# Kernel optimization log

Hardware: AMD Instinct MI355X
Metric: run time of the kernel (lower is better)

The kernel has to match this reference:

```python
import jax, jax.numpy as jnp
import numpy as np

N_NODES = 100000
N_EDGES = 1600000


def setup_inputs() -> dict:
    key = jax.random.key(0)
    k1, k2, k3, k4 = jax.random.split(key, 4)
    x = jax.random.normal(k1, (N_NODES, 16), dtype=jnp.float32)
    edge_index = jax.random.randint(k2, (2, N_EDGES), 0, N_NODES, dtype=jnp.int32)
    # Glorot-ish init for the two GCN layers
    W1 = jax.random.normal(k3, (16, 32), dtype=jnp.float32) * (1.0 / np.sqrt(16))
    b1 = jnp.zeros((32,), dtype=jnp.float32)
    W2 = jax.random.normal(k4, (32, 2), dtype=jnp.float32) * (1.0 / np.sqrt(32))
    b2 = jnp.zeros((2,), dtype=jnp.float32)
    return {"x": x, "edge_index": edge_index, "W1": W1, "b1": b1, "W2": W2, "b2": b2}


def _gcn_conv(x, W, b, src, dst, norm, n_nodes):
    # PyG GCNConv: h = X @ W; aggregate norm * h[src] at dst; add bias.
    h = x @ W                                   # [N, out]
    msg = h[src] * norm[:, None]                # [E+N, out] gather + scale
    out = jax.ops.segment_sum(msg, dst, num_segments=n_nodes)
    return out + b


def reference(x, edge_index, W1, b1, W2, b2):
    n = x.shape[0]
    self_loops = jnp.arange(n, dtype=edge_index.dtype)
    src = jnp.concatenate([edge_index[0], self_loops])  # [E+N]
    dst = jnp.concatenate([edge_index[1], self_loops])
    # Symmetric GCN normalization: deg computed on graph with self-loops
    deg = jax.ops.segment_sum(jnp.ones_like(dst, dtype=x.dtype), dst, num_segments=n)
    dis = jnp.where(deg > 0, jax.lax.rsqrt(deg), 0.0)   # deg^{-1/2}
    norm = dis[src] * dis[dst]                          # [E+N]

    h = jax.nn.relu(_gcn_conv(x, W1, b1, src, dst, norm, n))
    out = _gcn_conv(h, W2, b2, src, dst, norm, n)
    return out
```

## Files before the change

### kernel.cpp

```cpp
#include <hip/hip_runtime.h>
#include <hip/hip_fp16.h>

static constexpr int N  = 100000;
static constexpr int E  = 1600000;
static constexpr int B  = 256;
static constexpr int BG = 512;

static constexpr int BC     = 1024;
static constexpr int NBLKC  = 256;
static constexpr int CHUNKC = E / NBLKC;
static constexpr int PERC   = (CHUNKC + BC - 1) / BC;
static constexpr int NBUCK  = (N + 127) / 128;
static constexpr int SLAB   = 3072;
static constexpr int GCS    = 16;


__global__ __launch_bounds__(BC) void kC_scatter(
        const int* __restrict__ src, const int* __restrict__ dst,
        int* __restrict__ gcur, int* __restrict__ gslab) {
    __shared__ int lhist[NBUCK];
    __shared__ int lbase[NBUCK];
    __shared__ int gb[NBUCK];
    __shared__ int wsum[16];
    __shared__ int stage[CHUNKC];

    int t = threadIdx.x, blk = blockIdx.x;
    for (int i = t; i < NBUCK; i += BC) lhist[i] = 0;
    __syncthreads();

    int eb = blk * CHUNKC;
    int ds[PERC], ss[PERC];
#pragma unroll
    for (int k = 0; k < PERC; ++k) {
        int idx = k * BC + t;
        if (idx < CHUNKC) {
            ds[k] = dst[eb + idx];
            ss[k] = src[eb + idx];
            atomicAdd(&lhist[ds[k] >> 7], 1);
        }
    }
    __syncthreads();

    int lane = t & 63, wv = t >> 6;
    int val = (t < NBUCK) ? lhist[t] : 0;
    int inc = val;
#pragma unroll
    for (int off = 1; off < 64; off <<= 1) {
        int u = __shfl_up(inc, off, 64);
        if (lane >= off) inc += u;
    }
    if (lane == 63) wsum[wv] = inc;
    __syncthreads();
    if (wv == 0) {
        int wval = (lane < 16) ? wsum[lane] : 0;
        int winc = wval;
#pragma unroll
        for (int off = 1; off < 16; off <<= 1) {
            int u = __shfl_up(winc, off, 64);
            if (lane >= off) winc += u;
        }
        if (lane < 16) wsum[lane] = winc - wval;
    }
    __syncthreads();
    if (t < NBUCK) lbase[t] = wsum[wv] + inc - val;
    __syncthreads();

    if (t < NBUCK) {
        int h = lhist[t];
        if (h > 0) gb[t] = t * SLAB + atomicAdd(&gcur[t * GCS], h);
        lhist[t] = 0;
    }
    __syncthreads();

#pragma unroll
    for (int k = 0; k < PERC; ++k) {
        int idx = k * BC + t;
        if (idx < CHUNKC) {
            int d = ds[k], b = d >> 7;
            int r = atomicAdd(&lhist[b], 1);
            stage[lbase[b] + r] = ss[k] | ((d & 127) << 17);
        }
    }
    __syncthreads();

    if (t < NBUCK) {
        int len = lhist[t];
        if (len > 0) {
            int s0 = lbase[t];
            int g  = gb[t];
            int cap = (t + 1) * SLAB - g;
            if (cap < 0) cap = 0;
            if (len > cap) len = cap;
            for (int i = 0; i < len; ++i) gslab[g + i] = stage[s0 + i];
        }
    }
}


__global__ void kD1_deg(const int* __restrict__ gcur, const int* __restrict__ gslab,
                        int* __restrict__ rofs, const float4* __restrict__ x4,
                        __half* __restrict__ xpre) {
    __shared__ int c[128];
    __shared__ int wq[2];
    int t = threadIdx.x, b = blockIdx.x;
    if (t < 128) c[t] = 0;
    __syncthreads();

    int ne = min(gcur[b * GCS], SLAB);
    int base = b * SLAB;
    int ne4 = ne & ~3;
    for (int k = 4 * t; k < ne4; k += 4 * B) {
        int4 p4 = *(const int4*)(gslab + base + k);
        atomicAdd(&c[p4.x >> 17], 1);
        atomicAdd(&c[p4.y >> 17], 1);
        atomicAdd(&c[p4.z >> 17], 1);
        atomicAdd(&c[p4.w >> 17], 1);
    }
    if (t < ne - ne4) atomicAdd(&c[gslab[base + ne4 + t] >> 17], 1);
    __syncthreads();

    int lane = t & 63, wv = t >> 6;
    int val = (t < 128) ? c[t] : 0;
    int inc = val;
#pragma unroll
    for (int off = 1; off < 64; off <<= 1) {
        int u = __shfl_up(inc, off, 64);
        if (lane >= off) inc += u;
    }
    if (t == 63) wq[0] = inc;
    __syncthreads();
    if (t < 128) rofs[b * 129 + t] = base + inc - val + ((wv == 1) ? wq[0] : 0);
    if (t == 128) rofs[b * 129 + 128] = base + ne;

    int n = b * 128 + (t >> 1), h = t & 1;
    if (n < N) {
        float d = rsqrtf((float)(c[t >> 1] + 1));
        float4 u0 = x4[(size_t)n * 4 + h * 2];
        float4 u1 = x4[(size_t)n * 4 + h * 2 + 1];
        ushort4 p0, p1;
        p0.x = __half_as_ushort(__float2half(u0.x * d));
        p0.y = __half_as_ushort(__float2half(u0.y * d));
        p0.z = __half_as_ushort(__float2half(u0.z * d));
        p0.w = __half_as_ushort(__float2half(u0.w * d));
        p1.x = __half_as_ushort(__float2half(u1.x * d));
        p1.y = __half_as_ushort(__float2half(u1.y * d));
        p1.z = __half_as_ushort(__float2half(u1.z * d));
        p1.w = __half_as_ushort(__float2half(u1.w * d));
        *(ushort4*)(xpre + (size_t)n * 16 + h * 8)     = p0;
        *(ushort4*)(xpre + (size_t)n * 16 + h * 8 + 4) = p1;
    }
}


__global__ __launch_bounds__(BG) void kD2_agg(
        const __half* __restrict__ xpre, int* __restrict__ gslab,
        const int* __restrict__ rofs, const float* __restrict__ W1,
        const float* __restrict__ b1, const float* __restrict__ W2,
        float2* __restrict__ hpre) {
    __shared__ int st1[SLAB];
    __shared__ int cur[128];
    __shared__ int lofs[129];
    __shared__ float acc[128 * 17];
    __shared__ float sW1[512], sb1[32], sW2[64];
    int t = threadIdx.x, b = blockIdx.x;
    sW1[t] = W1[t];
    if (t < 32) sb1[t] = b1[t];
    if (t < 64) sW2[t] = W2[t];
    if (t < 128) cur[t] = 0;
    int base = b * SLAB;
    if (t < 129) lofs[t] = rofs[b * 129 + t] - base;
    __syncthreads();

    int ne = lofs[128];
    for (int k = t; k < ne; k += BG) {
        int p = gslab[base + k];
        int lo = p >> 17;
        int r = atomicAdd(&cur[lo], 1);
        st1[lofs[lo] + r] = p & 0x1FFFF;
    }
    __syncthreads();

    int ne4 = ne & ~3;
    for (int k = 4 * t; k < ne4; k += 4 * BG)
        *(int4*)(gslab + base + k) = *(const int4*)(st1 + k);
    for (int k = ne4 + t; k < ne; k += BG)
        gslab[base + k] = st1[k];

    int h = t & 1, e = (t >> 1) & 1, nl = t >> 2;
    int n = b * 128 + nl;
    float a0 = 0.f, a1 = 0.f, a2 = 0.f, a3 = 0.f,
          a4 = 0.f, a5 = 0.f, a6 = 0.f, a7 = 0.f;
    if (n < N) {
        auto add8 = [&](int4 w) {
            float2 q0 = __half22float2(*(__half2*)&w.x);
            float2 q1 = __half22float2(*(__half2*)&w.y);
            float2 q2 = __half22float2(*(__half2*)&w.z);
            float2 q3 = __half22float2(*(__half2*)&w.w);
            a0 += q0.x; a1 += q0.y; a2 += q1.x; a3 += q1.y;
            a4 += q2.x; a5 += q2.y; a6 += q3.x; a7 += q3.y;
        };
        int rs = lofs[nl], re = lofs[nl + 1];
        if (e == 0)
            add8(*(const int4*)(xpre + (size_t)n * 16 + h * 8));
        int k = rs + e;
        for (; k + 2 < re; k += 4) {
            int s0 = st1[k], s1 = st1[k + 2];
            int4 v0 = *(const int4*)(xpre + (size_t)s0 * 16 + h * 8);
            int4 v1 = *(const int4*)(xpre + (size_t)s1 * 16 + h * 8);
            add8(v0); add8(v1);
        }
        if (k < re)
            add8(*(const int4*)(xpre + (size_t)st1[k] * 16 + h * 8));
    }
    a0 += __shfl_xor(a0, 2, 64); a1 += __shfl_xor(a1, 2, 64);
    a2 += __shfl_xor(a2, 2, 64); a3 += __shfl_xor(a3, 2, 64);
    a4 += __shfl_xor(a4, 2, 64); a5 += __shfl_xor(a5, 2, 64);
    a6 += __shfl_xor(a6, 2, 64); a7 += __shfl_xor(a7, 2, 64);
    if (n < N && e == 0) {
        float* row = acc + nl * 17 + h * 8;
        row[0] = a0; row[1] = a1; row[2] = a2; row[3] = a3;
        row[4] = a4; row[5] = a5; row[6] = a6; row[7] = a7;
    }
    __syncthreads();

    if (t < 128) {
        int n2 = b * 128 + t;
        if (n2 < N) {
            int deg = lofs[t + 1] - lofs[t];
            float d = rsqrtf((float)(deg + 1));
            const float* row = acc + t * 17;
            float xi[16];
#pragma unroll
            for (int k = 0; k < 16; ++k) xi[k] = row[k] * d;
            float o0 = 0.f, o1 = 0.f;
#pragma unroll
            for (int c = 0; c < 32; ++c) {
                float hh = sb1[c];
#pragma unroll
                for (int k = 0; k < 16; ++k) hh = fmaf(xi[k], sW1[k * 32 + c], hh);
                hh = fmaxf(hh, 0.f);
                o0 = fmaf(hh, sW2[c * 2 + 0], o0);
                o1 = fmaf(hh, sW2[c * 2 + 1], o1);
            }
            hpre[n2] = make_float2(d * o0, d * o1);
        }
    }
}


__global__ __launch_bounds__(BG) void kF_l2(
        const float2* __restrict__ hpre, const int* __restrict__ gslab,
        const int* __restrict__ rofs, const float* __restrict__ b2,
        float2* __restrict__ out) {
    __shared__ int st1[SLAB];
    __shared__ int lofs[129];
    int t = threadIdx.x, b = blockIdx.x;
    int base = b * SLAB;
    if (t < 129) lofs[t] = rofs[b * 129 + t] - base;
    __syncthreads();

    int ne = lofs[128];
    int ne4 = ne & ~3;
    for (int k = 4 * t; k < ne4; k += 4 * BG)
        *(int4*)(st1 + k) = *(const int4*)(gslab + base + k);
    for (int k = ne4 + t; k < ne; k += BG)
        st1[k] = gslab[base + k];
    __syncthreads();

    int e = t & 3, nl = t >> 2;
    int n = b * 128 + nl;
    float o0 = 0.f, o1 = 0.f;
    int deg = 0;
    if (n < N) {
        int rs = lofs[nl], re = lofs[nl + 1];
        deg = re - rs;
        if (e == 0) {
            float2 self = hpre[n];
            o0 = self.x; o1 = self.y;
        }
        int k = rs + e;
        for (; k + 4 < re; k += 8) {
            float2 v0 = hpre[st1[k]];
            float2 v1 = hpre[st1[k + 4]];
            o0 += v0.x + v1.x;
            o1 += v0.y + v1.y;
        }
        if (k < re) {
            float2 v = hpre[st1[k]];
            o0 += v.x; o1 += v.y;
        }
    }
    o0 += __shfl_xor(o0, 1, 64); o1 += __shfl_xor(o1, 1, 64);
    o0 += __shfl_xor(o0, 2, 64); o1 += __shfl_xor(o1, 2, 64);
    if (n < N && e == 0) {
        float d = rsqrtf((float)(deg + 1));
        out[n] = make_float2(fmaf(d, o0, b2[0]), fmaf(d, o1, b2[1]));
    }
}


extern "C" void kernel_launch(void* const* d_in, const int* in_sizes, int n_in,
                              void* d_out, int out_size, void* d_ws, size_t ws_size,
                              hipStream_t stream) {
    const float* x  = (const float*)d_in[0];
    const int*   ei = (const int*)d_in[1];
    const float* W1 = (const float*)d_in[2];
    const float* b1 = (const float*)d_in[3];
    const float* W2 = (const float*)d_in[4];
    const float* b2 = (const float*)d_in[5];

    const int* src = ei;
    const int* dst = ei + E;

    int*    gslab = (int*)d_ws;
    int*    rofs  = gslab + (size_t)NBUCK * SLAB;
    int*    gcur  = rofs + 100880;
    float*  hpre  = (float*)(gcur + 12512);
    __half* xpre  = (__half*)(hpre + 2 * (size_t)N);

    hipMemsetAsync(gcur, 0, NBUCK * GCS * sizeof(int), stream);
    kC_scatter<<<NBLKC, BC, 0, stream>>>(src, dst, gcur, gslab);
    kD1_deg<<<NBUCK, B, 0, stream>>>(gcur, gslab, rofs, (const float4*)x, xpre);
    kD2_agg<<<NBUCK, BG, 0, stream>>>(xpre, gslab, rofs, W1, b1, W2, (float2*)hpre);
    kF_l2<<<NBUCK, BG, 0, stream>>>((const float2*)hpre, gslab, rofs, b2,
                                    (float2*)d_out);
}
```

Before: 128.9 us.

## Compute degrees via global atomics in scatter and simplify scan kernel

The scatter kernel now also counts per-node in-degree with global atomics, so the second kernel no longer rereads the slabs to build a per-bucket histogram. It only scans the precomputed degrees and writes the prescaled fp16 features, one thread per node. The scatter grid doubles to 512 blocks with an occupancy hint, and the two aggregation loops are unrolled further to keep more gathers in flight. The cost is 1.6M global atomics on random addresses plus a larger memset, and the memset now clears the degree array that is laid out right after gcur.

```diff
diff --git a/kernel.cpp b/kernel.cpp
--- a/kernel.cpp
+++ b/kernel.cpp
@@ -3,11 +3,11 @@
 
 static constexpr int N  = 100000;
 static constexpr int E  = 1600000;
-static constexpr int B  = 256;
+static constexpr int B1 = 128;
 static constexpr int BG = 512;
 
 static constexpr int BC     = 1024;
-static constexpr int NBLKC  = 256;
+static constexpr int NBLKC  = 512;
 static constexpr int CHUNKC = E / NBLKC;
 static constexpr int PERC   = (CHUNKC + BC - 1) / BC;
 static constexpr int NBUCK  = (N + 127) / 128;
@@ -15,9 +15,10 @@
 static constexpr int GCS    = 16;
 
 
-__global__ __launch_bounds__(BC) void kC_scatter(
+__global__ __launch_bounds__(BC, 8) void kC_scatter(
         const int* __restrict__ src, const int* __restrict__ dst,
-        int* __restrict__ gcur, int* __restrict__ gslab) {
+        int* __restrict__ gcur, int* __restrict__ gslab,
+        int* __restrict__ deg) {
     __shared__ int lhist[NBUCK];
     __shared__ int lbase[NBUCK];
     __shared__ int gb[NBUCK];
@@ -37,6 +38,7 @@
             ds[k] = dst[eb + idx];
             ss[k] = src[eb + idx];
             atomicAdd(&lhist[ds[k] >> 7], 1);
+            atomicAdd(&deg[ds[k]], 1);
         }
     }
     __syncthreads();
@@ -97,47 +99,35 @@
 }
 
 
-__global__ void kD1_deg(const int* __restrict__ gcur, const int* __restrict__ gslab,
-                        int* __restrict__ rofs, const float4* __restrict__ x4,
-                        __half* __restrict__ xpre) {
-    __shared__ int c[128];
-    __shared__ int wq[2];
+__global__ __launch_bounds__(B1) void kD1_scan(
+        const int* __restrict__ deg, int* __restrict__ rofs,
+        const float4* __restrict__ x4, __half* __restrict__ xpre) {
+    __shared__ int wq;
     int t = threadIdx.x, b = blockIdx.x;
-    if (t < 128) c[t] = 0;
-    __syncthreads();
-
-    int ne = min(gcur[b * GCS], SLAB);
-    int base = b * SLAB;
-    int ne4 = ne & ~3;
-    for (int k = 4 * t; k < ne4; k += 4 * B) {
-        int4 p4 = *(const int4*)(gslab + base + k);
-        atomicAdd(&c[p4.x >> 17], 1);
-        atomicAdd(&c[p4.y >> 17], 1);
-        atomicAdd(&c[p4.z >> 17], 1);
-        atomicAdd(&c[p4.w >> 17], 1);
-    }
-    if (t < ne - ne4) atomicAdd(&c[gslab[base + ne4 + t] >> 17], 1);
-    __syncthreads();
-
-    int lane = t & 63, wv = t >> 6;
-    int val = (t < 128) ? c[t] : 0;
-    int inc = val;
+    int n = b * 128 + t;
+    int dg = (n < N) ? deg[n] : 0;
+
+    int wv = t >> 6;
+    int inc = dg;
 #pragma unroll
     for (int off = 1; off < 64; off <<= 1) {
         int u = __shfl_up(inc, off, 64);
-        if (lane >= off) inc += u;
-    }
-    if (t == 63) wq[0] = inc;
-    __syncthreads();
-    if (t < 128) rofs[b * 129 + t] = base + inc - val + ((wv == 1) ? wq[0] : 0);
-    if (t == 128) rofs[b * 129 + 128] = base + ne;
-
-    int n = b * 128 + (t >> 1), h = t & 1;
+        if ((t & 63) >= off) inc += u;
+    }
+    if (t == 63) wq = inc;
+    __syncthreads();
+    int ex = inc - dg + ((wv == 1) ? wq : 0);
+    int base = b * SLAB;
+    rofs[b * 129 + t] = base + ex;
+    if (t == 127) rofs[b * 129 + 128] = base + ex + dg;
+
     if (n < N) {
-        float d = rsqrtf((float)(c[t >> 1] + 1));
-        float4 u0 = x4[(size_t)n * 4 + h * 2];
-        float4 u1 = x4[(size_t)n * 4 + h * 2 + 1];
-        ushort4 p0, p1;
+        float d = rsqrtf((float)(dg + 1));
+        float4 u0 = x4[(size_t)n * 4 + 0];
+        float4 u1 = x4[(size_t)n * 4 + 1];
+        float4 u2 = x4[(size_t)n * 4 + 2];
+        float4 u3 = x4[(size_t)n * 4 + 3];
+        ushort4 p0, p1, p2, p3;
         p0.x = __half_as_ushort(__float2half(u0.x * d));
         p0.y = __half_as_ushort(__float2half(u0.y * d));
         p0.z = __half_as_ushort(__float2half(u0.z * d));
@@ -146,8 +136,18 @@
         p1.y = __half_as_ushort(__float2half(u1.y * d));
         p1.z = __half_as_ushort(__float2half(u1.z * d));
         p1.w = __half_as_ushort(__float2half(u1.w * d));
-        *(ushort4*)(xpre + (size_t)n * 16 + h * 8)     = p0;
-        *(ushort4*)(xpre + (size_t)n * 16 + h * 8 + 4) = p1;
+        p2.x = __half_as_ushort(__float2half(u2.x * d));
+        p2.y = __half_as_ushort(__float2half(u2.y * d));
+        p2.z = __half_as_ushort(__float2half(u2.z * d));
+        p2.w = __half_as_ushort(__float2half(u2.w * d));
+        p3.x = __half_as_ushort(__float2half(u3.x * d));
+        p3.y = __half_as_ushort(__float2half(u3.y * d));
+        p3.z = __half_as_ushort(__float2half(u3.z * d));
+        p3.w = __half_as_ushort(__float2half(u3.w * d));
+        *(ushort4*)(xpre + (size_t)n * 16)      = p0;
+        *(ushort4*)(xpre + (size_t)n * 16 + 4)  = p1;
+        *(ushort4*)(xpre + (size_t)n * 16 + 8)  = p2;
+        *(ushort4*)(xpre + (size_t)n * 16 + 12) = p3;
     }
 }
 
@@ -203,13 +203,15 @@
         if (e == 0)
             add8(*(const int4*)(xpre + (size_t)n * 16 + h * 8));
         int k = rs + e;
-        for (; k + 2 < re; k += 4) {
-            int s0 = st1[k], s1 = st1[k + 2];
+        for (; k + 6 < re; k += 8) {
+            int s0 = st1[k], s1 = st1[k + 2], s2 = st1[k + 4], s3 = st1[k + 6];
             int4 v0 = *(const int4*)(xpre + (size_t)s0 * 16 + h * 8);
             int4 v1 = *(const int4*)(xpre + (size_t)s1 * 16 + h * 8);
-            add8(v0); add8(v1);
-        }
-        if (k < re)
+            int4 v2 = *(const int4*)(xpre + (size_t)s2 * 16 + h * 8);
+            int4 v3 = *(const int4*)(xpre + (size_t)s3 * 16 + h * 8);
+            add8(v0); add8(v1); add8(v2); add8(v3);
+        }
+        for (; k < re; k += 2)
             add8(*(const int4*)(xpre + (size_t)st1[k] * 16 + h * 8));
     }
     a0 += __shfl_xor(a0, 2, 64); a1 += __shfl_xor(a1, 2, 64);
@@ -279,13 +281,15 @@
             o0 = self.x; o1 = self.y;
         }
         int k = rs + e;
-        for (; k + 4 < re; k += 8) {
+        for (; k + 12 < re; k += 16) {
             float2 v0 = hpre[st1[k]];
             float2 v1 = hpre[st1[k + 4]];
-            o0 += v0.x + v1.x;
-            o1 += v0.y + v1.y;
-        }
-        if (k < re) {
+            float2 v2 = hpre[st1[k + 8]];
+            float2 v3 = hpre[st1[k + 12]];
+            o0 += (v0.x + v1.x) + (v2.x + v3.x);
+            o1 += (v0.y + v1.y) + (v2.y + v3.y);
+        }
+        for (; k < re; k += 4) {
             float2 v = hpre[st1[k]];
             o0 += v.x; o1 += v.y;
         }
@@ -315,12 +319,13 @@
     int*    gslab = (int*)d_ws;
     int*    rofs  = gslab + (size_t)NBUCK * SLAB;
     int*    gcur  = rofs + 100880;
-    float*  hpre  = (float*)(gcur + 12512);
+    int*    deg   = gcur + 12512;
+    float*  hpre  = (float*)(deg + 100000);
     __half* xpre  = (__half*)(hpre + 2 * (size_t)N);
 
-    hipMemsetAsync(gcur, 0, NBUCK * GCS * sizeof(int), stream);
-    kC_scatter<<<NBLKC, BC, 0, stream>>>(src, dst, gcur, gslab);
-    kD1_deg<<<NBUCK, B, 0, stream>>>(gcur, gslab, rofs, (const float4*)x, xpre);
+    hipMemsetAsync(gcur, 0, (NBUCK * GCS + N) * sizeof(int), stream);
+    kC_scatter<<<NBLKC, BC, 0, stream>>>(src, dst, gcur, gslab, deg);
+    kD1_scan<<<NBUCK, B1, 0, stream>>>(deg, rofs, (const float4*)x, xpre);
     kD2_agg<<<NBUCK, BG, 0, stream>>>(xpre, gslab, rofs, W1, b1, W2, (float2*)hpre);
     kF_l2<<<NBUCK, BG, 0, stream>>>((const float2*)hpre, gslab, rofs, b2,
                                     (float2*)d_out);
```

Measured after the change: 192.1 us. 1.49x slower.

## Scatter edges directly to global slabs and unroll gather loops deeper

Applied to the files above, without the earlier changes.

The bucketing kernel no longer stages edges in shared memory behind a block-wide prefix scan. Each edge now takes its rank from a shared-memory atomic and writes straight to its bucket slab, and edge indices are loaded as int2 pairs. This removes the scan, a large shared buffer and the serial per-bucket copy loop, at the cost of scattered global writes. The layer-1 and layer-2 gather loops are unrolled to four independent loads per iteration to raise memory-level parallelism.

```diff
diff --git a/kernel.cpp b/kernel.cpp
--- a/kernel.cpp
+++ b/kernel.cpp
@@ -9,60 +9,35 @@
 static constexpr int BC     = 1024;
 static constexpr int NBLKC  = 256;
 static constexpr int CHUNKC = E / NBLKC;
-static constexpr int PERC   = (CHUNKC + BC - 1) / BC;
+static constexpr int CH2    = CHUNKC / 2;
+static constexpr int PER2   = (CH2 + BC - 1) / BC;
 static constexpr int NBUCK  = (N + 127) / 128;
 static constexpr int SLAB   = 3072;
 static constexpr int GCS    = 16;
 
 
 __global__ __launch_bounds__(BC) void kC_scatter(
-        const int* __restrict__ src, const int* __restrict__ dst,
+        const int2* __restrict__ src2, const int2* __restrict__ dst2,
         int* __restrict__ gcur, int* __restrict__ gslab) {
     __shared__ int lhist[NBUCK];
-    __shared__ int lbase[NBUCK];
     __shared__ int gb[NBUCK];
-    __shared__ int wsum[16];
-    __shared__ int stage[CHUNKC];
 
     int t = threadIdx.x, blk = blockIdx.x;
     for (int i = t; i < NBUCK; i += BC) lhist[i] = 0;
     __syncthreads();
 
-    int eb = blk * CHUNKC;
-    int ds[PERC], ss[PERC];
-#pragma unroll
-    for (int k = 0; k < PERC; ++k) {
+    int eb2 = blk * CH2;
+    int2 dsv[PER2], ssv[PER2];
+#pragma unroll
+    for (int k = 0; k < PER2; ++k) {
         int idx = k * BC + t;
-        if (idx < CHUNKC) {
-            ds[k] = dst[eb + idx];
-            ss[k] = src[eb + idx];
-            atomicAdd(&lhist[ds[k] >> 7], 1);
-        }
-    }
-    __syncthreads();
-
-    int lane = t & 63, wv = t >> 6;
-    int val = (t < NBUCK) ? lhist[t] : 0;
-    int inc = val;
-#pragma unroll
-    for (int off = 1; off < 64; off <<= 1) {
-        int u = __shfl_up(inc, off, 64);
-        if (lane >= off) inc += u;
-    }
-    if (lane == 63) wsum[wv] = inc;
-    __syncthreads();
-    if (wv == 0) {
-        int wval = (lane < 16) ? wsum[lane] : 0;
-        int winc = wval;
-#pragma unroll
-        for (int off = 1; off < 16; off <<= 1) {
-            int u = __shfl_up(winc, off, 64);
-            if (lane >= off) winc += u;
-        }
-        if (lane < 16) wsum[lane] = winc - wval;
-    }
-    __syncthreads();
-    if (t < NBUCK) lbase[t] = wsum[wv] + inc - val;
+        if (idx < CH2) {
+            dsv[k] = dst2[eb2 + idx];
+            ssv[k] = src2[eb2 + idx];
+            atomicAdd(&lhist[dsv[k].x >> 7], 1);
+            atomicAdd(&lhist[dsv[k].y >> 7], 1);
+        }
+    }
     __syncthreads();
 
     if (t < NBUCK) {
@@ -73,25 +48,23 @@
     __syncthreads();
 
 #pragma unroll
-    for (int k = 0; k < PERC; ++k) {
+    for (int k = 0; k < PER2; ++k) {
         int idx = k * BC + t;
-        if (idx < CHUNKC) {
-            int d = ds[k], b = d >> 7;
-            int r = atomicAdd(&lhist[b], 1);
-            stage[lbase[b] + r] = ss[k] | ((d & 127) << 17);
-        }
-    }
-    __syncthreads();
-
-    if (t < NBUCK) {
-        int len = lhist[t];
-        if (len > 0) {
-            int s0 = lbase[t];
-            int g  = gb[t];
-            int cap = (t + 1) * SLAB - g;
-            if (cap < 0) cap = 0;
-            if (len > cap) len = cap;
-            for (int i = 0; i < len; ++i) gslab[g + i] = stage[s0 + i];
+        if (idx < CH2) {
+            {
+                int d = dsv[k].x, b = d >> 7;
+                int r = atomicAdd(&lhist[b], 1);
+                int g = gb[b] + r;
+                if (g < (b + 1) * SLAB)
+                    gslab[g] = ssv[k].x | ((d & 127) << 17);
+            }
+            {
+                int d = dsv[k].y, b = d >> 7;
+                int r = atomicAdd(&lhist[b], 1);
+                int g = gb[b] + r;
+                if (g < (b + 1) * SLAB)
+                    gslab[g] = ssv[k].y | ((d & 127) << 17);
+            }
         }
     }
 }
@@ -203,13 +176,15 @@
         if (e == 0)
             add8(*(const int4*)(xpre + (size_t)n * 16 + h * 8));
         int k = rs + e;
-        for (; k + 2 < re; k += 4) {
-            int s0 = st1[k], s1 = st1[k + 2];
+        for (; k + 6 < re; k += 8) {
+            int s0 = st1[k], s1 = st1[k + 2], s2 = st1[k + 4], s3 = st1[k + 6];
             int4 v0 = *(const int4*)(xpre + (size_t)s0 * 16 + h * 8);
             int4 v1 = *(const int4*)(xpre + (size_t)s1 * 16 + h * 8);
-            add8(v0); add8(v1);
-        }
-        if (k < re)
+            int4 v2 = *(const int4*)(xpre + (size_t)s2 * 16 + h * 8);
+            int4 v3 = *(const int4*)(xpre + (size_t)s3 * 16 + h * 8);
+            add8(v0); add8(v1); add8(v2); add8(v3);
+        }
+        for (; k < re; k += 2)
             add8(*(const int4*)(xpre + (size_t)st1[k] * 16 + h * 8));
     }
     a0 += __shfl_xor(a0, 2, 64); a1 += __shfl_xor(a1, 2, 64);
@@ -279,13 +254,15 @@
             o0 = self.x; o1 = self.y;
         }
         int k = rs + e;
-        for (; k + 4 < re; k += 8) {
+        for (; k + 12 < re; k += 16) {
             float2 v0 = hpre[st1[k]];
             float2 v1 = hpre[st1[k + 4]];
-            o0 += v0.x + v1.x;
-            o1 += v0.y + v1.y;
-        }
-        if (k < re) {
+            float2 v2 = hpre[st1[k + 8]];
+            float2 v3 = hpre[st1[k + 12]];
+            o0 += (v0.x + v1.x) + (v2.x + v3.x);
+            o1 += (v0.y + v1.y) + (v2.y + v3.y);
+        }
+        for (; k < re; k += 4) {
             float2 v = hpre[st1[k]];
             o0 += v.x; o1 += v.y;
         }
@@ -309,8 +286,8 @@
     const float* W2 = (const float*)d_in[4];
     const float* b2 = (const float*)d_in[5];
 
-    const int* src = ei;
-    const int* dst = ei + E;
+    const int2* src2 = (const int2*)ei;
+    const int2* dst2 = (const int2*)(ei + E);
 
     int*    gslab = (int*)d_ws;
     int*    rofs  = gslab + (size_t)NBUCK * SLAB;
@@ -319,7 +296,7 @@
     __half* xpre  = (__half*)(hpre + 2 * (size_t)N);
 
     hipMemsetAsync(gcur, 0, NBUCK * GCS * sizeof(int), stream);
-    kC_scatter<<<NBLKC, BC, 0, stream>>>(src, dst, gcur, gslab);
+    kC_scatter<<<NBLKC, BC, 0, stream>>>(src2, dst2, gcur, gslab);
     kD1_deg<<<NBUCK, B, 0, stream>>>(gcur, gslab, rofs, (const float4*)x, xpre);
     kD2_agg<<<NBUCK, BG, 0, stream>>>(xpre, gslab, rofs, W1, b1, W2, (float2*)hpre);
     kF_l2<<<NBUCK, BG, 0, stream>>>((const float2*)hpre, gslab, rofs, b2,
```

Result: no change. 129.0 us (median of 2 runs) (+0.0%).
